# Kernel optimization log

Measured on AMD Instinct MI355X. Metric: run time of the kernel, lower is better.

The kernel has to match this reference:

```python
import jax, jax.numpy as jnp
import numpy as np
from jax import lax

B, T, D, H = 256, 512, 128, 256  # batch, seq_len, input_dim, hidden_dim


def _lstm_layer(x_seq, Wih, Whh, bih, bhh):
    """Single PyTorch-convention LSTM layer. x_seq: [B,T,Din] -> [B,T,H].
    Gate order i, f, g, o; h0 = c0 = 0."""
    Bsz = x_seq.shape[0]
    Hd = Whh.shape[1]
    # Precompute input contributions for all timesteps: [B,T,4H]
    xg = jnp.einsum('btd,gd->btg', x_seq, Wih) + bih + bhh

    def step(carry, xg_t):
        h, c = carry
        gates = xg_t + h @ Whh.T  # [B,4H]
        i, f, g, o = jnp.split(gates, 4, axis=-1)
        i = jax.nn.sigmoid(i)
        f = jax.nn.sigmoid(f)
        g = jnp.tanh(g)
        o = jax.nn.sigmoid(o)
        c = f * c + i * g
        h = o * jnp.tanh(c)
        return (h, c), h

    init = (jnp.zeros((Bsz, Hd), x_seq.dtype), jnp.zeros((Bsz, Hd), x_seq.dtype))
    _, hs = lax.scan(step, init, jnp.swapaxes(xg, 0, 1))  # hs: [T,B,H]
    return jnp.swapaxes(hs, 0, 1)


def setup_inputs() -> dict:
    key = jax.random.key(0)
    ks = jax.random.split(key, 12)
    x = jax.random.normal(ks[0], (B, T, D), dtype=jnp.float32)
    # Left-contiguous mask: lengths in [1, T] (pack_padded_sequence semantics)
    lengths = jax.random.randint(ks[1], (B,), 1, T + 1)
    mask = (jnp.arange(T)[None, :] < lengths[:, None]).astype(jnp.int32)
    s0 = 1.0 / np.sqrt(H)
    u = lambda k, shape: jax.random.uniform(k, shape, jnp.float32, -s0, s0)
    return {
        'x': x,
        'mask': mask,
        'W_ih0': u(ks[2], (4 * H, D)),
        'W_hh0': u(ks[3], (4 * H, H)),
        'b_ih0': u(ks[4], (4 * H,)),
        'b_hh0': u(ks[5], (4 * H,)),
        'W_ih1': u(ks[6], (4 * H, H)),
        'W_hh1': u(ks[7], (4 * H, H)),
        'b_ih1': u(ks[8], (4 * H,)),
        'b_hh1': u(ks[9], (4 * H,)),
        'fc_w': u(ks[10], (1, H)),
        'fc_b': u(ks[11], (1,)),
    }


def reference(x, mask, W_ih0, W_hh0, b_ih0, b_hh0, W_ih1, W_hh1, b_ih1, b_hh1, fc_w, fc_b):
    # 2-layer LSTM (dropout inactive at inference)
    h1 = _lstm_layer(x, W_ih0, W_hh0, b_ih0, b_hh0)   # [B,T,H]
    h2 = _lstm_layer(h1, W_ih1, W_hh1, b_ih1, b_hh1)  # [B,T,H]
    # Gather output at last valid timestep per sequence (== packed result)
    lens = jnp.sum(mask, axis=1)                      # [B]
    last = h2[jnp.arange(h2.shape[0]), lens - 1]      # [B,H]
    return last @ fc_w.T + fc_b                       # [B,1]
```

## Files before the change

### kernel.cpp

```cpp
#include <hip/hip_runtime.h>
#include <stdint.h>

#define B_ 256
#define T_ 512
#define D_ 128
#define H_ 256

typedef __attribute__((ext_vector_type(8))) _Float16 half8;
typedef __attribute__((ext_vector_type(4))) float f32x4;
typedef __attribute__((ext_vector_type(4))) int i32x4;

#define WS_PART 0
#define WS_H0   65536
#define WS_H1   (65536 + 2*B_*H_*4)

__device__ __forceinline__ float fast_sig(float x) {
    return 1.0f / (1.0f + __expf(-x));
}
__device__ __forceinline__ float fast_tanh(float x) {
    float xc = fminf(fmaxf(x, -30.0f), 30.0f);
    float e = __expf(-2.0f * xc);
    return (1.0f - e) / (1.0f + e);
}
__device__ __forceinline__ half8 cvt8(const float* p) {
    const f32x4* q = (const f32x4*)p;
    f32x4 a = q[0], b = q[1];
    half8 r;
    r[0] = (_Float16)a[0]; r[1] = (_Float16)a[1];
    r[2] = (_Float16)a[2]; r[3] = (_Float16)a[3];
    r[4] = (_Float16)b[0]; r[5] = (_Float16)b[1];
    r[6] = (_Float16)b[2]; r[7] = (_Float16)b[3];
    return r;
}
__device__ __forceinline__ half8 cvt8v(f32x4 a, f32x4 b) {
    half8 r;
    r[0] = (_Float16)a[0]; r[1] = (_Float16)a[1];
    r[2] = (_Float16)a[2]; r[3] = (_Float16)a[3];
    r[4] = (_Float16)b[0]; r[5] = (_Float16)b[1];
    r[6] = (_Float16)b[2]; r[7] = (_Float16)b[3];
    return r;
}

__device__ __forceinline__ void bar_lds() {
    asm volatile("s_waitcnt lgkmcnt(0)" ::: "memory");
    __builtin_amdgcn_s_barrier();
}

__device__ __forceinline__ void poll4_issue(const unsigned* p, i32x4* r) {
    asm volatile(
        "global_load_dwordx4 %0, %4, off sc0 sc1\n\t"
        "global_load_dwordx4 %1, %4, off offset:16 sc0 sc1\n\t"
        "global_load_dwordx4 %2, %4, off offset:128 sc0 sc1\n\t"
        "global_load_dwordx4 %3, %4, off offset:144 sc0 sc1"
        : "=&v"(r[0]), "=&v"(r[1]), "=&v"(r[2]), "=&v"(r[3])
        : "v"(p) : "memory");
}
__device__ __forceinline__ void poll4_wait(const unsigned* p, i32x4* r) {
    asm volatile(
        "global_load_dwordx4 %0, %4, off sc0 sc1\n\t"
        "global_load_dwordx4 %1, %4, off offset:16 sc0 sc1\n\t"
        "global_load_dwordx4 %2, %4, off offset:128 sc0 sc1\n\t"
        "global_load_dwordx4 %3, %4, off offset:144 sc0 sc1\n\t"
        "s_waitcnt vmcnt(0)"
        : "=&v"(r[0]), "=&v"(r[1]), "=&v"(r[2]), "=&v"(r[3])
        : "v"(p) : "memory");
}
__device__ __forceinline__ void wait_tie8(i32x4* a, i32x4* b) {
    asm volatile("s_waitcnt vmcnt(0)"
        : "+v"(a[0]), "+v"(a[1]), "+v"(a[2]), "+v"(a[3]),
          "+v"(b[0]), "+v"(b[1]), "+v"(b[2]), "+v"(b[3]) :: "memory");
}
__device__ __forceinline__ void wait_tie4(i32x4* a) {
    asm volatile("s_waitcnt vmcnt(0)"
        : "+v"(a[0]), "+v"(a[1]), "+v"(a[2]), "+v"(a[3]) :: "memory");
}
__device__ __forceinline__ void store_dw_mall(unsigned* p, unsigned v) {
    asm volatile("global_store_dword %0, %1, off sc0 sc1" :: "v"(p), "v"(v) : "memory");
}

__device__ __forceinline__ int tags_ok(const i32x4* r, unsigned tag) {
    unsigned m = 0;
#pragma unroll
    for (int i = 0; i < 4; ++i) {
        m |= ((unsigned)r[i][0] ^ tag); m |= ((unsigned)r[i][1] ^ tag);
        m |= ((unsigned)r[i][2] ^ tag); m |= ((unsigned)r[i][3] ^ tag);
    }
    return __all((m & 0xFFFF0000u) == 0);
}
__device__ __forceinline__ void unpack_to_lds(const i32x4* r, _Float16* base) {
#pragma unroll
    for (int t = 0; t < 2; ++t) {
        i32x4 pk;
        pk[0] = (r[2 * t][0] & 0xFFFF) | (r[2 * t][1] << 16);
        pk[1] = (r[2 * t][2] & 0xFFFF) | (r[2 * t][3] << 16);
        pk[2] = (r[2 * t + 1][0] & 0xFFFF) | (r[2 * t + 1][1] << 16);
        pk[3] = (r[2 * t + 1][2] & 0xFFFF) | (r[2 * t + 1][3] << 16);
        *(i32x4*)(base + t * 32) = pk;
    }
}

__global__ __launch_bounds__(256, 1) void lstm_main(
    const float* __restrict__ x, const int* __restrict__ mask,
    const float* __restrict__ Wih0, const float* __restrict__ Whh0,
    const float* __restrict__ bih0, const float* __restrict__ bhh0,
    const float* __restrict__ Wih1, const float* __restrict__ Whh1,
    const float* __restrict__ bih1, const float* __restrict__ bhh1,
    const float* __restrict__ fcw, char* __restrict__ ws)
{
    const int tid  = threadIdx.x;
    const int blk  = blockIdx.x;
    const int g    = blk & 15;
    const int sl   = blk >> 4;
    const int b0   = g * 16;
    const int j0   = sl * 16;
    const int w    = tid >> 6;
    const int lane = tid & 63;
    const int row  = lane & 15;
    const int quad = lane >> 4;
    const int kb   = quad * 8;

    float*    partials = (float*)(ws + WS_PART);
    unsigned* h0u      = (unsigned*)(ws + WS_H0);
    unsigned* h1u      = (unsigned*)(ws + WS_H1);

    __shared__ float gbuf[2048];
    __shared__ __align__(16) _Float16 hsh0[16 * 264];
    __shared__ __align__(16) _Float16 hsh1[16 * 264];

    const int n = w * H_ + j0 + row;
    half8 wA[12], wB[16];
#pragma unroll
    for (int kt = 0; kt < 4; ++kt) wA[kt]     = cvt8(&Wih0[(size_t)n * D_ + kt * 32 + kb]);
#pragma unroll
    for (int kt = 0; kt < 8; ++kt) wA[4 + kt] = cvt8(&Whh0[(size_t)n * H_ + kt * 32 + kb]);
#pragma unroll
    for (int kt = 0; kt < 8; ++kt) wB[kt]     = cvt8(&Wih1[(size_t)n * H_ + kt * 32 + kb]);
#pragma unroll
    for (int kt = 0; kt < 8; ++kt) wB[8 + kt] = cvt8(&Whh1[(size_t)n * H_ + kt * 32 + kb]);
    const float biasA = bih0[n] + bhh0[n];
    const float biasB = bih1[n] + bhh1[n];

    const int bb    = tid >> 4;
    const int jj    = tid & 15;
    const int bglob = b0 + bb;

    int len = 0;
    {
        const int* mrow = mask + (size_t)bglob * T_ + jj * 32;
#pragma unroll
        for (int q = 0; q < 32; ++q) len += mrow[q];
#pragma unroll
        for (int o = 1; o < 16; o <<= 1) len += __shfl_xor(len, o, 16);
    }

    float c0 = 0.f, c1 = 0.f, hsave = 0.f;

    const float* xrow = x + (size_t)(b0 + row) * T_ * D_ + kb;
    f32x4 xacc = {0.f, 0.f, 0.f, 0.f};
#pragma unroll
    for (int kt = 0; kt < 4; ++kt)
        xacc = __builtin_amdgcn_mfma_f32_16x16x32_f16(cvt8(xrow + kt * 32), wA[kt], xacc, 0, 0, 0);

    i32x4 r0[4], r1[4];
    const int koff = w * 64 + quad * 8;

    for (int u = 0; u <= T_; ++u) {
        half8 a0[8], a1[8];
        f32x4 xr[8];
        int h1ok = 1;
        const unsigned tag1 = (unsigned)(u - 1) << 16;
        const unsigned* p1 = h1u + ((size_t)(u & 1) * B_ + (b0 + row)) * H_ + koff;

        if (u >= 1) {
            wait_tie8(r0, r1);
            const unsigned tag0 = (unsigned)u << 16;
            const unsigned* p0 = h0u + ((size_t)((u - 1) & 1) * B_ + (b0 + row)) * H_ + koff;
            int guard = 0;
            while (!tags_ok(r0, tag0)) {
                poll4_wait(p0, r0);
                if (++guard > (1 << 15)) break;
            }
            h1ok = (u >= 2) ? tags_ok(r1, tag1) : 1;
            if (u >= 2 && !h1ok) poll4_issue(p1, r1);
            {
                const int tn = (u + 1 < T_) ? (u + 1) : (T_ - 1);
                const f32x4* q = (const f32x4*)(xrow + (size_t)tn * D_);
#pragma unroll
                for (int kt = 0; kt < 4; ++kt) { xr[2 * kt] = q[kt * 8]; xr[2 * kt + 1] = q[kt * 8 + 1]; }
            }
            unpack_to_lds(r0, hsh0 + row * 264 + koff);
            bar_lds();
#pragma unroll
            for (int kt = 0; kt < 8; ++kt)
                a0[kt] = *(const half8*)(hsh0 + row * 264 + kt * 32 + quad * 8);
        } else {
            const f32x4* q = (const f32x4*)(xrow + (size_t)1 * D_);
#pragma unroll
            for (int kt = 0; kt < 4; ++kt) { xr[2 * kt] = q[kt * 8]; xr[2 * kt + 1] = q[kt * 8 + 1]; }
        }

        if (u < T_) {
            f32x4 acc0 = xacc;
            if (u >= 1) {
#pragma unroll
                for (int kt = 0; kt < 8; ++kt)
                    acc0 = __builtin_amdgcn_mfma_f32_16x16x32_f16(a0[kt], wA[4 + kt], acc0, 0, 0, 0);
            }
#pragma unroll
            for (int r = 0; r < 4; ++r)
                gbuf[w * 256 + (quad * 4 + r) * 16 + row] = acc0[r] + biasA;
            bar_lds();
            const int idx = bb * 16 + jj;
            float gi = fast_sig(gbuf[idx]);
            float gf = fast_sig(gbuf[256 + idx]);
            float gg = fast_tanh(gbuf[512 + idx]);
            float go = fast_sig(gbuf[768 + idx]);
            c0 = gf * c0 + gi * gg;
            float h0v = go * fast_tanh(c0);
            union { _Float16 h; unsigned short s; } cv; cv.h = (_Float16)h0v;
            store_dw_mall(h0u + ((size_t)(u & 1) * B_ + bglob) * H_ + j0 + jj,
                          ((unsigned)(u + 1) << 16) | cv.s);
        }
        __builtin_amdgcn_sched_barrier(0);

        if (u >= 1) {
            f32x4 acc1 = {0.f, 0.f, 0.f, 0.f};
#pragma unroll
            for (int kt = 0; kt < 8; ++kt)
                acc1 = __builtin_amdgcn_mfma_f32_16x16x32_f16(a0[kt], wB[kt], acc1, 0, 0, 0);
            if (u >= 2) {
                if (!h1ok) {
                    wait_tie4(r1);
                    h1ok = tags_ok(r1, tag1);
                    int guard = 0;
                    while (!h1ok) {
                        poll4_wait(p1, r1);
                        h1ok = tags_ok(r1, tag1);
                        if (++guard > (1 << 15)) break;
                    }
                }
                unpack_to_lds(r1, hsh1 + row * 264 + koff);
                bar_lds();
#pragma unroll
                for (int kt = 0; kt < 8; ++kt)
                    a1[kt] = *(const half8*)(hsh1 + row * 264 + kt * 32 + quad * 8);
#pragma unroll
                for (int kt = 0; kt < 8; ++kt)
                    acc1 = __builtin_amdgcn_mfma_f32_16x16x32_f16(a1[kt], wB[8 + kt], acc1, 0, 0, 0);
            }
#pragma unroll
            for (int r = 0; r < 4; ++r)
                gbuf[1024 + w * 256 + (quad * 4 + r) * 16 + row] = acc1[r] + biasB;
            bar_lds();
            const int idx = bb * 16 + jj;
            float gi = fast_sig(gbuf[1024 + idx]);
            float gf = fast_sig(gbuf[1024 + 256 + idx]);
            float gg = fast_tanh(gbuf[1024 + 512 + idx]);
            float go = fast_sig(gbuf[1024 + 768 + idx]);
            c1 = gf * c1 + gi * gg;
            float h1v = go * fast_tanh(c1);
            union { _Float16 h; unsigned short s; } cv; cv.h = (_Float16)h1v;
            store_dw_mall(h1u + ((size_t)((u - 1) & 1) * B_ + bglob) * H_ + j0 + jj,
                          ((unsigned)u << 16) | cv.s);
            if (u == len) hsave = h1v;
        }

        if (u < T_) {
            const int v = u + 1;
            const unsigned* q0 = h0u + ((size_t)((v - 1) & 1) * B_ + (b0 + row)) * H_ + koff;
            const unsigned* q1 = (v >= 2)
                ? h1u + ((size_t)(v & 1) * B_ + (b0 + row)) * H_ + koff
                : q0;
            poll4_issue(q0, r0);
            poll4_issue(q1, r1);
        }

        if (u < T_ - 1) {
            f32x4 t = {0.f, 0.f, 0.f, 0.f};
#pragma unroll
            for (int kt = 0; kt < 4; ++kt)
                t = __builtin_amdgcn_mfma_f32_16x16x32_f16(cvt8v(xr[2 * kt], xr[2 * kt + 1]), wA[kt], t, 0, 0, 0);
            xacc = t;
        }
    }

    float part = hsave * fcw[j0 + jj];
#pragma unroll
    for (int o = 1; o < 16; o <<= 1) part += __shfl_xor(part, o, 16);
    if (jj == 0) partials[sl * B_ + bglob] = part;
}

__global__ void lstm_fc(const float* __restrict__ fcb, const char* __restrict__ ws,
                        float* __restrict__ out) {
    const int b = threadIdx.x;
    const float* partials = (const float*)(ws + WS_PART);
    float s = fcb[0];
#pragma unroll
    for (int sl = 0; sl < 16; ++sl) s += partials[sl * B_ + b];
    out[b] = s;
}

extern "C" void kernel_launch(void* const* d_in, const int* in_sizes, int n_in,
                              void* d_out, int out_size, void* d_ws, size_t ws_size,
                              hipStream_t stream) {
    const float* xx    = (const float*)d_in[0];
    const int*   mask  = (const int*)d_in[1];
    const float* Wih0  = (const float*)d_in[2];
    const float* Whh0  = (const float*)d_in[3];
    const float* bih0  = (const float*)d_in[4];
    const float* bhh0  = (const float*)d_in[5];
    const float* Wih1  = (const float*)d_in[6];
    const float* Whh1  = (const float*)d_in[7];
    const float* bih1  = (const float*)d_in[8];
    const float* bhh1  = (const float*)d_in[9];
    const float* fcw   = (const float*)d_in[10];
    const float* fcb   = (const float*)d_in[11];

    lstm_main<<<dim3(256), dim3(256), 0, stream>>>(
        xx, mask, Wih0, Whh0, bih0, bhh0, Wih1, Whh1, bih1, bhh1, fcw, (char*)d_ws);
    lstm_fc<<<dim3(1), dim3(256), 0, stream>>>(fcb, (const char*)d_ws, (float*)d_out);
}
```

Baseline: 1.715 ms.

## Add L2-scoped fast-path copy of hidden-state exchange buffers alongside system-coherent copy

```diff
diff --git a/kernel.cpp b/kernel.cpp
--- a/kernel.cpp
+++ b/kernel.cpp
@@ -12,7 +12,9 @@
 
 #define WS_PART 0
 #define WS_H0   65536
-#define WS_H1   (65536 + 2*B_*H_*4)
+#define WS_H1   (WS_H0 + 2*B_*H_*4)
+#define WS_F0   (WS_H1 + 2*B_*H_*4)
+#define WS_F1   (WS_F0 + 2*B_*H_*4)
 
 __device__ __forceinline__ float fast_sig(float x) {
     return 1.0f / (1.0f + __expf(-x));
@@ -46,15 +48,6 @@
     __builtin_amdgcn_s_barrier();
 }
 
-__device__ __forceinline__ void poll4_issue(const unsigned* p, i32x4* r) {
-    asm volatile(
-        "global_load_dwordx4 %0, %4, off sc0 sc1\n\t"
-        "global_load_dwordx4 %1, %4, off offset:16 sc0 sc1\n\t"
-        "global_load_dwordx4 %2, %4, off offset:128 sc0 sc1\n\t"
-        "global_load_dwordx4 %3, %4, off offset:144 sc0 sc1"
-        : "=&v"(r[0]), "=&v"(r[1]), "=&v"(r[2]), "=&v"(r[3])
-        : "v"(p) : "memory");
-}
 __device__ __forceinline__ void poll4_wait(const unsigned* p, i32x4* r) {
     asm volatile(
         "global_load_dwordx4 %0, %4, off sc0 sc1\n\t"
@@ -65,17 +58,37 @@
         : "=&v"(r[0]), "=&v"(r[1]), "=&v"(r[2]), "=&v"(r[3])
         : "v"(p) : "memory");
 }
+__device__ __forceinline__ void store_dw_mall(unsigned* p, unsigned v) {
+    asm volatile("global_store_dword %0, %1, off sc0 sc1" :: "v"(p), "v"(v) : "memory");
+}
+
+__device__ __forceinline__ void poll4f_issue(const unsigned* p, i32x4* r) {
+    asm volatile(
+        "global_load_dwordx4 %0, %4, off sc0\n\t"
+        "global_load_dwordx4 %1, %4, off offset:16 sc0\n\t"
+        "global_load_dwordx4 %2, %4, off offset:128 sc0\n\t"
+        "global_load_dwordx4 %3, %4, off offset:144 sc0"
+        : "=&v"(r[0]), "=&v"(r[1]), "=&v"(r[2]), "=&v"(r[3])
+        : "v"(p) : "memory");
+}
+__device__ __forceinline__ void poll4f_wait(const unsigned* p, i32x4* r) {
+    asm volatile(
+        "global_load_dwordx4 %0, %4, off sc0\n\t"
+        "global_load_dwordx4 %1, %4, off offset:16 sc0\n\t"
+        "global_load_dwordx4 %2, %4, off offset:128 sc0\n\t"
+        "global_load_dwordx4 %3, %4, off offset:144 sc0\n\t"
+        "s_waitcnt vmcnt(0)"
+        : "=&v"(r[0]), "=&v"(r[1]), "=&v"(r[2]), "=&v"(r[3])
+        : "v"(p) : "memory");
+}
+__device__ __forceinline__ void store_dw_l2(unsigned* p, unsigned v) {
+    asm volatile("global_store_dword %0, %1, off sc0" :: "v"(p), "v"(v) : "memory");
+}
+
 __device__ __forceinline__ void wait_tie8(i32x4* a, i32x4* b) {
     asm volatile("s_waitcnt vmcnt(0)"
         : "+v"(a[0]), "+v"(a[1]), "+v"(a[2]), "+v"(a[3]),
           "+v"(b[0]), "+v"(b[1]), "+v"(b[2]), "+v"(b[3]) :: "memory");
-}
-__device__ __forceinline__ void wait_tie4(i32x4* a) {
-    asm volatile("s_waitcnt vmcnt(0)"
-        : "+v"(a[0]), "+v"(a[1]), "+v"(a[2]), "+v"(a[3]) :: "memory");
-}
-__device__ __forceinline__ void store_dw_mall(unsigned* p, unsigned v) {
-    asm volatile("global_store_dword %0, %1, off sc0 sc1" :: "v"(p), "v"(v) : "memory");
 }
 
 __device__ __forceinline__ int tags_ok(const i32x4* r, unsigned tag) {
@@ -122,6 +135,8 @@
     float*    partials = (float*)(ws + WS_PART);
     unsigned* h0u      = (unsigned*)(ws + WS_H0);
     unsigned* h1u      = (unsigned*)(ws + WS_H1);
+    unsigned* f0u      = (unsigned*)(ws + WS_F0);
+    unsigned* f1u      = (unsigned*)(ws + WS_F1);
 
     __shared__ float gbuf[2048];
     __shared__ __align__(16) _Float16 hsh0[16 * 264];
@@ -169,19 +184,21 @@
         f32x4 xr[8];
         int h1ok = 1;
         const unsigned tag1 = (unsigned)(u - 1) << 16;
-        const unsigned* p1 = h1u + ((size_t)(u & 1) * B_ + (b0 + row)) * H_ + koff;
+        const size_t off1 = ((size_t)(u & 1) * B_ + (b0 + row)) * H_ + koff;
 
         if (u >= 1) {
             wait_tie8(r0, r1);
             const unsigned tag0 = (unsigned)u << 16;
-            const unsigned* p0 = h0u + ((size_t)((u - 1) & 1) * B_ + (b0 + row)) * H_ + koff;
-            int guard = 0;
-            while (!tags_ok(r0, tag0)) {
-                poll4_wait(p0, r0);
-                if (++guard > (1 << 15)) break;
+            const size_t off0 = ((size_t)((u - 1) & 1) * B_ + (b0 + row)) * H_ + koff;
+            if (!tags_ok(r0, tag0)) {
+                poll4f_wait(f0u + off0, r0);
+                int guard = 0;
+                while (!tags_ok(r0, tag0)) {
+                    poll4_wait(h0u + off0, r0);
+                    if (++guard > (1 << 15)) break;
+                }
             }
             h1ok = (u >= 2) ? tags_ok(r1, tag1) : 1;
-            if (u >= 2 && !h1ok) poll4_issue(p1, r1);
             {
                 const int tn = (u + 1 < T_) ? (u + 1) : (T_ - 1);
                 const f32x4* q = (const f32x4*)(xrow + (size_t)tn * D_);
@@ -218,8 +235,10 @@
             c0 = gf * c0 + gi * gg;
             float h0v = go * fast_tanh(c0);
             union { _Float16 h; unsigned short s; } cv; cv.h = (_Float16)h0v;
-            store_dw_mall(h0u + ((size_t)(u & 1) * B_ + bglob) * H_ + j0 + jj,
-                          ((unsigned)(u + 1) << 16) | cv.s);
+            const unsigned pv = ((unsigned)(u + 1) << 16) | cv.s;
+            const size_t so = ((size_t)(u & 1) * B_ + bglob) * H_ + j0 + jj;
+            store_dw_l2(f0u + so, pv);
+            store_dw_mall(h0u + so, pv);
         }
         __builtin_amdgcn_sched_barrier(0);
 
@@ -230,11 +249,11 @@
                 acc1 = __builtin_amdgcn_mfma_f32_16x16x32_f16(a0[kt], wB[kt], acc1, 0, 0, 0);
             if (u >= 2) {
                 if (!h1ok) {
-                    wait_tie4(r1);
+                    poll4f_wait(f1u + off1, r1);
                     h1ok = tags_ok(r1, tag1);
                     int guard = 0;
                     while (!h1ok) {
-                        poll4_wait(p1, r1);
+                        poll4_wait(h1u + off1, r1);
                         h1ok = tags_ok(r1, tag1);
                         if (++guard > (1 << 15)) break;
                     }
@@ -260,19 +279,21 @@
             c1 = gf * c1 + gi * gg;
             float h1v = go * fast_tanh(c1);
             union { _Float16 h; unsigned short s; } cv; cv.h = (_Float16)h1v;
-            store_dw_mall(h1u + ((size_t)((u - 1) & 1) * B_ + bglob) * H_ + j0 + jj,
-                          ((unsigned)u << 16) | cv.s);
+            const unsigned pv = ((unsigned)u << 16) | cv.s;
+            const size_t so = ((size_t)((u - 1) & 1) * B_ + bglob) * H_ + j0 + jj;
+            store_dw_l2(f1u + so, pv);
+            store_dw_mall(h1u + so, pv);
             if (u == len) hsave = h1v;
         }
 
         if (u < T_) {
             const int v = u + 1;
-            const unsigned* q0 = h0u + ((size_t)((v - 1) & 1) * B_ + (b0 + row)) * H_ + koff;
+            const unsigned* q0 = f0u + ((size_t)((v - 1) & 1) * B_ + (b0 + row)) * H_ + koff;
             const unsigned* q1 = (v >= 2)
-                ? h1u + ((size_t)(v & 1) * B_ + (b0 + row)) * H_ + koff
+                ? f1u + ((size_t)(v & 1) * B_ + (b0 + row)) * H_ + koff
                 : q0;
-            poll4_issue(q0, r0);
-            poll4_issue(q1, r1);
+            poll4f_issue(q0, r0);
+            poll4f_issue(q1, r1);
         }
 
         if (u < T_ - 1) {
```

After: 1.807 ms. 5.4% more time.
